# Kernel optimization log

Measured on AMD Instinct MI355X. Metric: run time of the kernel, lower is better.

Reference implementation:

```python
import jax, jax.numpy as jnp
import numpy as np

T, B, D, H = 1500, 16, 512, 1024
KEEP = 0.8        # 1 - dropout[i], scalar drop mask in test mode
BN_EPS = 1e-5     # torch BatchNorm1d default eps


def setup_inputs() -> dict:
    key = jax.random.key(0)
    ks = jax.random.split(key, 40)
    inp = {}
    inp['x'] = jax.random.normal(ks[0], (T, B, D), jnp.float32)
    inp['x_len'] = jax.random.randint(ks[1], (B,), 1, T + 1)
    dims_in = [D, H]
    ki = 2
    for i in range(2):
        din = dims_in[i]
        # xavier-ish feedforward weights, orthogonal-ish recurrent weights
        inp[f'wh_W{i}'] = jax.random.normal(ks[ki], (H, din), jnp.float32) / np.float32(np.sqrt(din)); ki += 1
        inp[f'wz_W{i}'] = jax.random.normal(ks[ki], (H, din), jnp.float32) / np.float32(np.sqrt(din)); ki += 1
        inp[f'uh_W{i}'] = jax.random.normal(ks[ki], (H, H), jnp.float32) / np.float32(np.sqrt(H)); ki += 1
        inp[f'uz_W{i}'] = jax.random.normal(ks[ki], (H, H), jnp.float32) / np.float32(np.sqrt(H)); ki += 1
        for tag in ('bnh', 'bnz'):
            inp[f'{tag}_g{i}'] = 1.0 + 0.1 * jax.random.normal(ks[ki], (H,), jnp.float32); ki += 1
            inp[f'{tag}_b{i}'] = 0.1 * jax.random.normal(ks[ki], (H,), jnp.float32); ki += 1
            inp[f'{tag}_m{i}'] = 0.1 * jax.random.normal(ks[ki], (H,), jnp.float32); ki += 1
            inp[f'{tag}_v{i}'] = jax.random.uniform(ks[ki], (H,), jnp.float32, 0.5, 1.5); ki += 1
    return inp


def _bn_eval(y, g, b, m, v):
    # eval-mode BatchNorm1d with running stats, applied over last dim
    return g * (y - m) / jnp.sqrt(v + BN_EPS) + b


def _ligru_layer(x, whW, wzW, uhW, uzW, bnh, bnz):
    # pre-scan input projections + batchnorm: [T, B, H]
    wh = _bn_eval(jnp.einsum('tbd,hd->tbh', x, whW), *bnh)
    wz = _bn_eval(jnp.einsum('tbd,hd->tbh', x, wzW), *bnz)

    def step(ht, wk):
        whk, wzk = wk  # [B, H]
        zt = jax.nn.sigmoid(wzk + ht @ uzW.T)
        at = whk + ht @ uhW.T
        hcand = jax.nn.relu(at) * KEEP
        ht = zt * ht + (1.0 - zt) * hcand
        return ht, ht

    h0 = jnp.zeros((x.shape[1], whW.shape[0]), x.dtype)
    _, h = jax.lax.scan(step, h0, (wh, wz))
    return h  # [T, B, H]


def reference(x, x_len,
              wh_W0, wz_W0, uh_W0, uz_W0,
              bnh_g0, bnh_b0, bnh_m0, bnh_v0,
              bnz_g0, bnz_b0, bnz_m0, bnz_v0,
              wh_W1, wz_W1, uh_W1, uz_W1,
              bnh_g1, bnh_b1, bnh_m1, bnh_v1,
              bnz_g1, bnz_b1, bnz_m1, bnz_v1):
    x = _ligru_layer(x, wh_W0, wz_W0, uh_W0, uz_W0,
                     (bnh_g0, bnh_b0, bnh_m0, bnh_v0),
                     (bnz_g0, bnz_b0, bnz_m0, bnz_v0))
    x = _ligru_layer(x, wh_W1, wz_W1, uh_W1, uz_W1,
                     (bnh_g1, bnh_b1, bnh_m1, bnh_v1),
                     (bnz_g1, bnz_b1, bnz_m1, bnz_v1))
    return (x, x_len)
```

## Files before the change

### kernel.cpp

```cpp
#include <hip/hip_runtime.h>
#include <math.h>

#define TT 1500
#define BB 16
#define HH 1024
#define MM (TT*BB)
#define KEEPF 0.8f
#define EPSF 1e-5f
#define NFLT ((size_t)MM * HH)

#define AGENT __HIP_MEMORY_SCOPE_AGENT
typedef unsigned long long u64;

__global__ __launch_bounds__(256) void gemm_bn_kernel(
    const float* __restrict__ A, int K,
    const float* __restrict__ Wh, const float* __restrict__ Wz,
    const float* __restrict__ bnh_g, const float* __restrict__ bnh_b,
    const float* __restrict__ bnh_m, const float* __restrict__ bnh_v,
    const float* __restrict__ bnz_g, const float* __restrict__ bnz_b,
    const float* __restrict__ bnz_m, const float* __restrict__ bnz_v,
    float* __restrict__ outh, float* __restrict__ outz)
{
    __shared__ float As[16][68];
    __shared__ float Ws[16][68];
    const int mb = blockIdx.x;
    const int nb = blockIdx.y;
    const int jbase = nb * 64;
    const bool isz = jbase >= 1024;
    const float* W = isz ? Wz : Wh;
    const int jloc = isz ? (jbase - 1024) : jbase;

    const int tid = threadIdx.x;
    const int r = tid >> 2, q = tid & 3;
    const int tm = tid & 15, tn = tid >> 4;

    float acc[4][4] = {};
    for (int kt = 0; kt < K; kt += 16) {
        float4 a = *(const float4*)(A + (size_t)(mb * 64 + r) * K + kt + q * 4);
        float4 w = *(const float4*)(W + (size_t)(jloc + r) * K + kt + q * 4);
        __syncthreads();
        As[q*4+0][r] = a.x; As[q*4+1][r] = a.y; As[q*4+2][r] = a.z; As[q*4+3][r] = a.w;
        Ws[q*4+0][r] = w.x; Ws[q*4+1][r] = w.y; Ws[q*4+2][r] = w.z; Ws[q*4+3][r] = w.w;
        __syncthreads();
        #pragma unroll
        for (int k = 0; k < 16; ++k) {
            float4 a4 = *(const float4*)(&As[k][tm * 4]);
            float4 w4 = *(const float4*)(&Ws[k][tn * 4]);
            float av[4] = {a4.x, a4.y, a4.z, a4.w};
            float wv[4] = {w4.x, w4.y, w4.z, w4.w};
            #pragma unroll
            for (int i = 0; i < 4; ++i)
                #pragma unroll
                for (int j = 0; j < 4; ++j)
                    acc[i][j] += av[i] * wv[j];
        }
    }

    const float* g = isz ? bnz_g : bnh_g;
    const float* b = isz ? bnz_b : bnh_b;
    const float* m = isz ? bnz_m : bnh_m;
    const float* v = isz ? bnz_v : bnh_v;
    float* outp = isz ? outz : outh;

    float sc[4], sh[4];
    #pragma unroll
    for (int j = 0; j < 4; ++j) {
        int jc = jloc + tn * 4 + j;
        float s = g[jc] * rsqrtf(v[jc] + EPSF);
        sc[j] = s;
        sh[j] = b[jc] - m[jc] * s;
    }
    #pragma unroll
    for (int i = 0; i < 4; ++i) {
        int mrow = mb * 64 + tm * 4 + i;
        float4 o;
        o.x = acc[i][0] * sc[0] + sh[0];
        o.y = acc[i][1] * sc[1] + sh[1];
        o.z = acc[i][2] * sc[2] + sh[2];
        o.w = acc[i][3] * sc[3] + sh[3];
        *(float4*)(outp + (size_t)mrow * HH + jloc + tn * 4) = o;
    }
}

__global__ __launch_bounds__(256, 1) void scan_kernel(
    const float* __restrict__ wh, const float* __restrict__ wz,
    const float* __restrict__ uh, const float* __restrict__ uz,
    float* __restrict__ hout, unsigned* __restrict__ cnt)
{
    const int tid  = threadIdx.x, bid = blockIdx.x;
    const int lane = tid & 63;
    const int ks   = lane & 31;
    const int mat  = lane >> 5;
    const int rg   = tid >> 6;
    const int j0   = bid * 4;
    const int row0 = rg * 4;

    const float* Um = mat ? uz : uh;
    float4 u[4][8];
    #pragma unroll
    for (int c = 0; c < 4; ++c) {
        const float* up = Um + (size_t)(j0 + c) * HH + 4 * ks;
        #pragma unroll
        for (int it = 0; it < 8; ++it)
            u[c][it] = *(const float4*)(up + 128 * it);
    }

    const bool g0 = (lane == 0);
    float hprev[4][4];
    #pragma unroll
    for (int r = 0; r < 4; ++r)
        #pragma unroll
        for (int c = 0; c < 4; ++c) hprev[r][c] = 0.f;

    unsigned want = 0;
    for (int t = 0; t < TT; ++t) {
        float4 whv[4], wzv[4];
        if (g0) {
            #pragma unroll
            for (int r = 0; r < 4; ++r) {
                const size_t base = ((size_t)t * BB + row0 + r) * HH + j0;
                whv[r] = *(const float4*)(wh + base);
                wzv[r] = *(const float4*)(wz + base);
            }
        }

        float acc[4][4] = {};
        if (t > 0) {
            int spins = 0;
            bool dead = false;
            while (!__all(__hip_atomic_load(cnt + ((lane & 7) << 5),
                                            __ATOMIC_RELAXED, AGENT) >= want)) {
                if (++spins > 4000000) { dead = true; break; }
                __builtin_amdgcn_s_sleep(2);
            }
            if (dead) break;
            asm volatile("" ::: "memory");

            const float* hb = hout + (size_t)(t - 1) * BB * HH;
            #pragma unroll
            for (int it = 0; it < 8; ++it) {
                #pragma unroll
                for (int r = 0; r < 4; ++r) {
                    const float4 hv = *(const float4*)(hb + (size_t)(row0 + r) * HH + 4 * ks + 128 * it);
                    #pragma unroll
                    for (int c = 0; c < 4; ++c)
                        acc[c][r] += hv.x * u[c][it].x + hv.y * u[c][it].y
                                   + hv.z * u[c][it].z + hv.w * u[c][it].w;
                }
            }
            #pragma unroll
            for (int d = 1; d < 32; d <<= 1)
                #pragma unroll
                for (int c = 0; c < 4; ++c)
                    #pragma unroll
                    for (int r = 0; r < 4; ++r)
                        acc[c][r] += __shfl_xor(acc[c][r], d, 64);
        }
        float zacc[4][4];
        #pragma unroll
        for (int c = 0; c < 4; ++c)
            #pragma unroll
            for (int r = 0; r < 4; ++r)
                zacc[c][r] = __shfl_xor(acc[c][r], 32, 64);

        if (g0) {
            #pragma unroll
            for (int r = 0; r < 4; ++r) {
                float hn[4];
                #pragma unroll
                for (int c = 0; c < 4; ++c) {
                    const float zt = 1.f / (1.f + __expf(-((&wzv[r].x)[c] + zacc[c][r])));
                    const float at = (&whv[r].x)[c] + acc[c][r];
                    const float hc = fmaxf(at, 0.f) * KEEPF;
                    hn[c] = zt * hprev[r][c] + (1.f - zt) * hc;
                    hprev[r][c] = hn[c];
                }
                u64* dst = (u64*)(hout + ((size_t)t * BB + row0 + r) * HH + j0);
                union { float f[2]; u64 v; } p0, p1;
                p0.f[0] = hn[0]; p0.f[1] = hn[1];
                p1.f[0] = hn[2]; p1.f[1] = hn[3];
                __hip_atomic_store(dst,     p0.v, __ATOMIC_RELAXED, AGENT);
                __hip_atomic_store(dst + 1, p1.v, __ATOMIC_RELAXED, AGENT);
            }
        }
        __syncthreads();
        if (tid == 0)
            __hip_atomic_fetch_add(cnt + ((bid >> 5) << 5), 1u, __ATOMIC_RELAXED, AGENT);
        want += 32;
    }
}

__global__ void lencopy_kernel(const int* __restrict__ xl, float* __restrict__ out) {
    int i = threadIdx.x;
    if (i < BB) out[i] = (float)xl[i];
}

extern "C" void kernel_launch(void* const* d_in, const int* in_sizes, int n_in,
                              void* d_out, int out_size, void* d_ws, size_t ws_size,
                              hipStream_t stream) {
    const float* x    = (const float*)d_in[0];
    const int*   xlen = (const int*)d_in[1];
    const float* whW0 = (const float*)d_in[2];
    const float* wzW0 = (const float*)d_in[3];
    const float* uhW0 = (const float*)d_in[4];
    const float* uzW0 = (const float*)d_in[5];
    const float* bnh0[4] = {(const float*)d_in[6], (const float*)d_in[7], (const float*)d_in[8], (const float*)d_in[9]};
    const float* bnz0[4] = {(const float*)d_in[10], (const float*)d_in[11], (const float*)d_in[12], (const float*)d_in[13]};
    const float* whW1 = (const float*)d_in[14];
    const float* wzW1 = (const float*)d_in[15];
    const float* uhW1 = (const float*)d_in[16];
    const float* uzW1 = (const float*)d_in[17];
    const float* bnh1[4] = {(const float*)d_in[18], (const float*)d_in[19], (const float*)d_in[20], (const float*)d_in[21]};
    const float* bnz1[4] = {(const float*)d_in[22], (const float*)d_in[23], (const float*)d_in[24], (const float*)d_in[25]};

    float* whb = (float*)d_ws;
    float* wzb = whb + NFLT;
    float* h0  = wzb + NFLT;
    unsigned* bar = (unsigned*)((char*)d_ws + 3 * NFLT * sizeof(float));
    float* out0 = (float*)d_out;

    hipMemsetAsync(bar, 0, 4096, stream);

    dim3 ggrid(MM / 64, 32), gblk(256);

    gemm_bn_kernel<<<ggrid, gblk, 0, stream>>>(
        x, 512, whW0, wzW0,
        bnh0[0], bnh0[1], bnh0[2], bnh0[3],
        bnz0[0], bnz0[1], bnz0[2], bnz0[3],
        whb, wzb);

    {
        const float* a0 = whb; const float* a1 = wzb;
        const float* a2 = uhW0; const float* a3 = uzW0;
        float* a4 = h0; unsigned* a5 = bar;
        void* args[] = {&a0, &a1, &a2, &a3, &a4, &a5};
        hipLaunchCooperativeKernel((const void*)scan_kernel, dim3(256), dim3(256), args, 0, stream);
    }

    gemm_bn_kernel<<<ggrid, gblk, 0, stream>>>(
        h0, 1024, whW1, wzW1,
        bnh1[0], bnh1[1], bnh1[2], bnh1[3],
        bnz1[0], bnz1[1], bnz1[2], bnz1[3],
        whb, wzb);

    {
        const float* a0 = whb; const float* a1 = wzb;
        const float* a2 = uhW1; const float* a3 = uzW1;
        float* a4 = out0; unsigned* a5 = bar + 256;
        void* args[] = {&a0, &a1, &a2, &a3, &a4, &a5};
        hipLaunchCooperativeKernel((const void*)scan_kernel, dim3(256), dim3(256), args, 0, stream);
    }

    lencopy_kernel<<<1, 64, 0, stream>>>(xlen, out0 + NFLT);
}
```

Measured before the change: 36.58 ms.

## Partition scan by batch groups with per-wave counters instead of global barrier

```diff
diff --git a/kernel.cpp b/kernel.cpp
--- a/kernel.cpp
+++ b/kernel.cpp
@@ -89,17 +89,19 @@
 {
     const int tid  = threadIdx.x, bid = blockIdx.x;
     const int lane = tid & 63;
+    const int wv   = tid >> 6;
     const int ks   = lane & 31;
     const int mat  = lane >> 5;
-    const int rg   = tid >> 6;
-    const int j0   = bid * 4;
-    const int row0 = rg * 4;
+    const int g    = bid >> 6;
+    const int ib   = bid & 63;
+    const int c0   = ib * 16 + wv * 4;
+    const int row0 = g * 4;
 
     const float* Um = mat ? uz : uh;
     float4 u[4][8];
     #pragma unroll
     for (int c = 0; c < 4; ++c) {
-        const float* up = Um + (size_t)(j0 + c) * HH + 4 * ks;
+        const float* up = Um + (size_t)(c0 + c) * HH + 4 * ks;
         #pragma unroll
         for (int it = 0; it < 8; ++it)
             u[c][it] = *(const float4*)(up + 128 * it);
@@ -112,13 +114,15 @@
         #pragma unroll
         for (int c = 0; c < 4; ++c) hprev[r][c] = 0.f;
 
-    unsigned want = 0;
+    unsigned* mycnt = cnt + ((unsigned)bid << 2);
+    const unsigned* gcnt = cnt + ((unsigned)(g * 64) << 2);
+
     for (int t = 0; t < TT; ++t) {
         float4 whv[4], wzv[4];
         if (g0) {
             #pragma unroll
             for (int r = 0; r < 4; ++r) {
-                const size_t base = ((size_t)t * BB + row0 + r) * HH + j0;
+                const size_t base = ((size_t)t * BB + row0 + r) * HH + c0;
                 whv[r] = *(const float4*)(wh + base);
                 wzv[r] = *(const float4*)(wz + base);
             }
@@ -126,12 +130,14 @@
 
         float acc[4][4] = {};
         if (t > 0) {
+            const unsigned want = 4u * (unsigned)t;
             int spins = 0;
             bool dead = false;
-            while (!__all(__hip_atomic_load(cnt + ((lane & 7) << 5),
-                                            __ATOMIC_RELAXED, AGENT) >= want)) {
+            unsigned v = __hip_atomic_load(gcnt + (lane << 2), __ATOMIC_RELAXED, AGENT);
+            while (!__all(v >= want)) {
                 if (++spins > 4000000) { dead = true; break; }
-                __builtin_amdgcn_s_sleep(2);
+                __builtin_amdgcn_s_sleep(4);
+                v = __hip_atomic_load(gcnt + (lane << 2), __ATOMIC_RELAXED, AGENT);
             }
             if (dead) break;
             asm volatile("" ::: "memory");
@@ -175,18 +181,16 @@
                     hn[c] = zt * hprev[r][c] + (1.f - zt) * hc;
                     hprev[r][c] = hn[c];
                 }
-                u64* dst = (u64*)(hout + ((size_t)t * BB + row0 + r) * HH + j0);
+                u64* dst = (u64*)(hout + ((size_t)t * BB + row0 + r) * HH + c0);
                 union { float f[2]; u64 v; } p0, p1;
                 p0.f[0] = hn[0]; p0.f[1] = hn[1];
                 p1.f[0] = hn[2]; p1.f[1] = hn[3];
                 __hip_atomic_store(dst,     p0.v, __ATOMIC_RELAXED, AGENT);
                 __hip_atomic_store(dst + 1, p1.v, __ATOMIC_RELAXED, AGENT);
             }
-        }
-        __syncthreads();
-        if (tid == 0)
-            __hip_atomic_fetch_add(cnt + ((bid >> 5) << 5), 1u, __ATOMIC_RELAXED, AGENT);
-        want += 32;
+            asm volatile("s_waitcnt vmcnt(0)" ::: "memory");
+            __hip_atomic_fetch_add(mycnt, 1u, __ATOMIC_RELAXED, AGENT);
+        }
     }
 }
 
@@ -216,10 +220,11 @@
     float* whb = (float*)d_ws;
     float* wzb = whb + NFLT;
     float* h0  = wzb + NFLT;
-    unsigned* bar = (unsigned*)((char*)d_ws + 3 * NFLT * sizeof(float));
+    unsigned* cnt0 = (unsigned*)((char*)d_ws + 3 * NFLT * sizeof(float));
+    unsigned* cnt1 = cnt0 + 1024;
     float* out0 = (float*)d_out;
 
-    hipMemsetAsync(bar, 0, 4096, stream);
+    hipMemsetAsync(cnt0, 0, 8192, stream);
 
     dim3 ggrid(MM / 64, 32), gblk(256);
 
@@ -232,7 +237,7 @@
     {
         const float* a0 = whb; const float* a1 = wzb;
         const float* a2 = uhW0; const float* a3 = uzW0;
-        float* a4 = h0; unsigned* a5 = bar;
+        float* a4 = h0; unsigned* a5 = cnt0;
         void* args[] = {&a0, &a1, &a2, &a3, &a4, &a5};
         hipLaunchCooperativeKernel((const void*)scan_kernel, dim3(256), dim3(256), args, 0, stream);
     }
@@ -246,7 +251,7 @@
     {
         const float* a0 = whb; const float* a1 = wzb;
         const float* a2 = uhW1; const float* a3 = uzW1;
-        float* a4 = out0; unsigned* a5 = bar + 256;
+        float* a4 = out0; unsigned* a5 = cnt1;
         void* args[] = {&a0, &a1, &a2, &a3, &a4, &a5};
         hipLaunchCooperativeKernel((const void*)scan_kernel, dim3(256), dim3(256), args, 0, stream);
     }
```

Measured after the change: 32.94 ms. -9.9%, faster.
